# Optimization experiments

Hardware: AMD Instinct MI355X
Metric: run time of the kernel (lower is better)

Reference implementation:

```python
import jax, jax.numpy as jnp
import numpy as np

IN_CH, OUT_CH, K, STRIDE, PAD = 256, 256, 3, 1, 1

# Straight-through-estimator sign (torch Binarize: sign fwd, identity bwd)
@jax.custom_vjp
def ste_sign(x):
    return jnp.sign(x)

def _ste_fwd(x):
    return jnp.sign(x), None

def _ste_bwd(_, g):
    return (g,)

ste_sign.defvjp(_ste_fwd, _ste_bwd)


def setup_inputs() -> dict:
    key = jax.random.key(0)
    ks = jax.random.split(key, 4)
    x = jax.random.normal(ks[0], (32, IN_CH, 56, 56), jnp.float32)
    shift1 = jnp.zeros((1, IN_CH, 1, 1), jnp.float32)
    shift2 = jnp.zeros((1, IN_CH, 1, 1), jnp.float32)
    fan_in = IN_CH * K * K
    weight = jax.random.normal(ks[1], (OUT_CH, IN_CH, K, K), jnp.float32) / np.sqrt(fan_in)
    bias = jax.random.normal(ks[2], (OUT_CH,), jnp.float32) * 0.01
    w1 = jax.random.uniform(ks[3], (1,), jnp.float32) * 0.001  # channel_w scalar
    return {"x": x, "shift1": shift1, "shift2": shift2,
            "weight": weight, "bias": bias, "w1": w1}


def _binarize_conv2d(x, weight, bias):
    # BinarizeConv2d: binarize input (in_ch != 3) and weight via sign, fp conv, add bias
    xb = ste_sign(x)
    wb = ste_sign(weight)
    out = jax.lax.conv_general_dilated(
        xb, wb,
        window_strides=(STRIDE, STRIDE),
        padding=[(PAD, PAD), (PAD, PAD)],
        dimension_numbers=("NCHW", "OIHW", "NCHW"))
    return out + bias[None, :, None, None]


def reference(x, shift1, shift2, weight, bias, w1):
    out1 = _binarize_conv2d(x + shift1, weight, bias)
    out2 = _binarize_conv2d(x + shift2, weight, bias)
    return out1 + w1 * out2
```

## Files before the change

### kernel.cpp

```cpp
#include <hip/hip_runtime.h>
#include <stdint.h>

typedef __attribute__((ext_vector_type(4))) int   i32x4v;
typedef __attribute__((ext_vector_type(16))) int  i32x16v;
typedef __attribute__((ext_vector_type(4))) float f32x4;

#define PIX 3136
#define WW 56
#define SPL 53824
#define SLAB 215296
#define ABUF 16384
#define EPQ (32*69*4)
#define LDSB 65536

#define XBP_BYTES ((size_t)32*4*215296)
#define OFF_XBP2  (XBP_BYTES)
#define OFF_WBT   (2*XBP_BYTES)
#define WBT_BYTES ((size_t)9*16*256*16)
#define OFF_FLAG  (OFF_WBT + WBT_BYTES)
#define WS_NEED   (OFF_FLAG + 64)

__global__ __launch_bounds__(256) void k_prep(
    const float* __restrict__ s1, const float* __restrict__ s2,
    const float* __restrict__ w, char* __restrict__ ws,
    char* __restrict__ wbTt, int* __restrict__ flag) {
    int b = blockIdx.x;
    int t = threadIdx.x;
    if (b == 0) {
        __shared__ int bad;
        if (t == 0) bad = 0;
        __syncthreads();
        if (s1[t] != s2[t]) atomicAdd(&bad, 1);
        __syncthreads();
        if (t == 0) *flag = (bad == 0) ? 1 : 0;
        return;
    }
    if (b <= 256) {
        char* base = ws + (size_t)(b - 1) * SLAB;
        int4 z = {0, 0, 0, 0};
#pragma unroll
        for (int i = 0; i < 4; ++i) {
            int u = t + i * 256;
            if (u >= 912) break;
            int s = u / 228, v = u - s * 228;
            int off;
            if (v < 58)       off = v;
            else if (v < 116) off = 3306 + (v - 58);
            else { int r = v - 116; off = ((r >> 1) + 1) * 58 + (r & 1) * 57; }
            *(int4*)(base + s * SPL + off * 16) = z;
        }
        return;
    }
    int idx = (b - 257) * 256 + t;
    int kk = idx >> 16;
    int sub = (idx >> 12) & 15;
    int oc = (idx >> 4) & 255;
    int lo = idx & 15;
    float v = w[(oc * 256 + sub * 16 + lo) * 9 + kk];
    wbTt[idx] = (v > 0.f) ? (char)1 : ((v < 0.f) ? (char)-1 : (char)0);
}

__global__ __launch_bounds__(256) void k_repack_x(
    const float* __restrict__ x, const float* __restrict__ sh1,
    const float* __restrict__ sh2, char* __restrict__ xbp1,
    char* __restrict__ xbp2, const int* __restrict__ flag) {
    __shared__ float lds[64 * 68];
    bool eq = (*flag != 0);
    int t = threadIdx.x;
    int b = blockIdx.x;
    int n = b / 49;
    int p0 = (b % 49) * 64;

    int pixw = t >> 2;
    int sub  = t & 3;
    int pw = p0 + pixw;
    int yw = pw / WW, xw = pw % WW;

    int cl = t >> 4;
    int p4 = (t & 15) * 4;

    for (int cc = 0; cc < 256; cc += 64) {
        __syncthreads();
#pragma unroll
        for (int i = 0; i < 4; ++i) {
            float4 v = *(const float4*)(x + (size_t)(n * 256 + cc + cl + i * 16) * PIX + p0 + p4);
            *(float4*)(&lds[(cl + i * 16) * 68 + p4]) = v;
        }
        __syncthreads();
        size_t obase = (size_t)(n * 4 + (cc >> 6)) * SLAB + (size_t)sub * SPL
                     + ((size_t)(yw + 1) * 58 + (xw + 1)) * 16;
        union { char c[16]; int4 v; } u1, u2;
#pragma unroll
        for (int k = 0; k < 16; ++k) {
            int c = sub * 16 + k;
            float v = lds[c * 68 + pixw];
            float a1 = v + sh1[cc + c];
            float a2 = v + sh2[cc + c];
            u1.c[k] = (a1 > 0.f) ? (char)1 : ((a1 < 0.f) ? (char)-1 : (char)0);
            u2.c[k] = (a2 > 0.f) ? (char)1 : ((a2 < 0.f) ? (char)-1 : (char)0);
        }
        *(int4*)(xbp1 + obase) = u1.v;
        if (!eq) *(int4*)(xbp2 + obase) = u2.v;
    }
}

template <int MODE>
__global__ __launch_bounds__(256, 2) void k_bgemm(
    const char* __restrict__ xsrc, const char* __restrict__ wbTt,
    const float* __restrict__ bias, const float* __restrict__ w1,
    const int* __restrict__ flag, float* __restrict__ out) {
    bool eq = (*flag != 0);
    if (MODE == 0 ? !eq : eq) return;

    __shared__ char lds[LDSB];

    int t = threadIdx.x;
    int l = t & 63, wid = t >> 6;
    int r32 = l & 31, half = l >> 5;

    int logical = (blockIdx.x & 7) * 196 + (blockIdx.x >> 3);
    int n = logical / 49, tp = logical % 49;
    int p0 = tp * 64;
    int y0 = p0 / WW;
    int ocw = wid * 64;

    int wpm[2];
#pragma unroll
    for (int mi = 0; mi < 2; ++mi) {
        int g = p0 + mi * 32 + r32;
        int yg = g / WW, xg = g - yg * WW;
        wpm[mi] = (yg + 1 - y0) * 58 + xg + 1;
    }

    auto stageB = [&](int par, int t2) {
        const int cc2 = t2 / 9, kk2 = t2 % 9;
        const char* src = wbTt + kk2 * 65536 + cc2 * 16384 + wid * 4096 + l * 16;
        char* dst = lds + 32768 + par * 16384 + wid * 4096;
#pragma unroll
        for (int j = 0; j < 4; ++j)
            __builtin_amdgcn_global_load_lds(
                (const __attribute__((address_space(1))) void*)(src + j * 1024),
                (__attribute__((address_space(3))) void*)(dst + j * 1024), 16, 0, 0);
    };
    auto stageA = [&](int par, int cc2) {
        const char* src = xsrc + (size_t)(n * 4 + cc2) * SLAB + (size_t)wid * SPL
                        + y0 * 928 + l * 16;
        char* dst = lds + par * ABUF + wid * 4096;
#pragma unroll
        for (int j = 0; j < 4; ++j)
            __builtin_amdgcn_global_load_lds(
                (const __attribute__((address_space(1))) void*)(src + j * 1024),
                (__attribute__((address_space(3))) void*)(dst + j * 1024), 16, 0, 0);
    };

    i32x16v acc[2][2];
#pragma unroll
    for (int mi = 0; mi < 2; ++mi)
#pragma unroll
        for (int nj = 0; nj < 2; ++nj)
#pragma unroll
            for (int i = 0; i < 16; ++i) acc[mi][nj][i] = 0;

    stageA(0, 0);
    stageB(0, 0);
    __syncthreads();

#pragma unroll
    for (int tix = 0; tix < 36; ++tix) {
        const int cc = tix / 9, kk = tix % 9;
        if (tix < 35) stageB((tix + 1) & 1, tix + 1);
        if (kk == 4 && cc < 3) stageA((cc + 1) & 1, cc + 1);
        const int ts = (kk / 3 - 1) * 58 + (kk % 3) - 1;
        const char* Ab = lds + (cc & 1) * ABUF;
        const char* Bb = lds + 32768 + (tix & 1) * 16384;
#pragma unroll
        for (int kq = 0; kq < 2; ++kq) {
            const int ci = kq * 2 + half;
            i32x4v af0 = *(const i32x4v*)(Ab + ci * 4096 + (wpm[0] + ts) * 16);
            i32x4v af1 = *(const i32x4v*)(Ab + ci * 4096 + (wpm[1] + ts) * 16);
            i32x4v bf0 = *(const i32x4v*)(Bb + ci * 4096 + (ocw + r32) * 16);
            i32x4v bf1 = *(const i32x4v*)(Bb + ci * 4096 + (ocw + 32 + r32) * 16);
            acc[0][0] = __builtin_amdgcn_mfma_i32_32x32x32_i8(af0, bf0, acc[0][0], 0, 0, 0);
            acc[0][1] = __builtin_amdgcn_mfma_i32_32x32x32_i8(af0, bf1, acc[0][1], 0, 0, 0);
            acc[1][0] = __builtin_amdgcn_mfma_i32_32x32x32_i8(af1, bf0, acc[1][0], 0, 0, 0);
            acc[1][1] = __builtin_amdgcn_mfma_i32_32x32x32_i8(af1, bf1, acc[1][1], 0, 0, 0);
        }
        __syncthreads();
    }

    float w1v = w1[0];
    float se = 1.f + w1v;
    float* sb = (float*)(lds + wid * EPQ);
    size_t outb = (size_t)n * 256 * PIX + p0;

#pragma unroll
    for (int nj = 0; nj < 2; ++nj) {
        float bv = bias[ocw + nj * 32 + r32];
#pragma unroll
        for (int mi = 0; mi < 2; ++mi)
#pragma unroll
            for (int q = 0; q < 4; ++q) {
                f32x4 v;
#pragma unroll
                for (int j = 0; j < 4; ++j) {
                    float a = (float)(acc[mi][nj][q * 4 + j]);
                    if (MODE == 0)      v[j] = (a + bv) * se;
                    else if (MODE == 1) v[j] = a + se * bv;
                    else                v[j] = w1v * a;
                }
                *(f32x4*)(sb + r32 * 69 + mi * 32 + q * 8 + half * 4) = v;
            }
        asm volatile("s_waitcnt lgkmcnt(0)" ::: "memory");
#pragma unroll
        for (int p = 0; p < 8; ++p) {
            int row = p * 4 + (l >> 4);
            int px4 = (l & 15) * 4;
            f32x4 v = *(const f32x4*)(sb + row * 69 + px4);
            float* op = out + outb + (size_t)(ocw + nj * 32 + row) * PIX + px4;
            if (MODE == 2) {
                f32x4 o = *(const f32x4*)op;
                v[0] += o[0]; v[1] += o[1]; v[2] += o[2]; v[3] += o[3];
            }
            __builtin_nontemporal_store(v, (f32x4*)op);
        }
        if (nj == 0) asm volatile("s_waitcnt lgkmcnt(0)" ::: "memory");
    }
}

extern "C" void kernel_launch(void* const* d_in, const int* in_sizes, int n_in,
                              void* d_out, int out_size, void* d_ws, size_t ws_size,
                              hipStream_t stream) {
    const float* x    = (const float*)d_in[0];
    const float* sh1  = (const float*)d_in[1];
    const float* sh2  = (const float*)d_in[2];
    const float* wgt  = (const float*)d_in[3];
    const float* bias = (const float*)d_in[4];
    const float* w1   = (const float*)d_in[5];
    float* out = (float*)d_out;
    char* ws = (char*)d_ws;
    if (ws_size < WS_NEED) return;

    char* xbp1 = ws;
    char* xbp2 = ws + OFF_XBP2;
    char* wbTt = ws + OFF_WBT;
    int* flag  = (int*)(ws + OFF_FLAG);

    k_prep<<<2561, 256, 0, stream>>>(sh1, sh2, wgt, ws, wbTt, flag);
    k_repack_x<<<32 * 49, 256, 0, stream>>>(x, sh1, sh2, xbp1, xbp2, flag);
    k_bgemm<0><<<1568, 256, 0, stream>>>(xbp1, wbTt, bias, w1, flag, out);
    k_bgemm<1><<<1568, 256, 0, stream>>>(xbp1, wbTt, bias, w1, flag, out);
    k_bgemm<2><<<1568, 256, 0, stream>>>(xbp2, wbTt, bias, w1, flag, out);
}
```

Before: 116.6 us.

## Retile binary conv GEMM to 128px x 128oc blocks with single A buffer

Changes the block tile from 64 pixels x 256 output channels to 128 pixels x 128 channels, with 4 waves arranged 2x2, and uses 1600 blocks with clamped tails. The A (input) slab is now single-buffered and reloaded between channel chunks behind an extra barrier. B staging is halved, so LDS per block falls to about 37KB, which lets launch bounds target 3 blocks per CU. The aim is higher occupancy and better reuse balance, at the cost of exposed A-load latency at each chunk boundary and some wasted work on the padded last pixel tile.

Result: faster. 105.5 us (-9.6%).

```diff
diff --git a/kernel.cpp b/kernel.cpp
--- a/kernel.cpp
+++ b/kernel.cpp
@@ -9,9 +9,10 @@
 #define WW 56
 #define SPL 53824
 #define SLAB 215296
-#define ABUF 16384
+#define APL 5184
+#define ABASE 16384
 #define EPQ (32*69*4)
-#define LDSB 65536
+#define LDSB 37120
 
 #define XBP_BYTES ((size_t)32*4*215296)
 #define OFF_XBP2  (XBP_BYTES)
@@ -105,7 +106,7 @@
 }
 
 template <int MODE>
-__global__ __launch_bounds__(256, 2) void k_bgemm(
+__global__ __launch_bounds__(256, 3) void k_bgemm(
     const char* __restrict__ xsrc, const char* __restrict__ wbTt,
     const float* __restrict__ bias, const float* __restrict__ w1,
     const int* __restrict__ flag, float* __restrict__ out) {
@@ -116,38 +117,46 @@
 
     int t = threadIdx.x;
     int l = t & 63, wid = t >> 6;
+    int wr = wid >> 1, wc = wid & 1;
     int r32 = l & 31, half = l >> 5;
 
-    int logical = (blockIdx.x & 7) * 196 + (blockIdx.x >> 3);
-    int n = logical / 49, tp = logical % 49;
-    int p0 = tp * 64;
+    int logical = (blockIdx.x & 7) * 200 + (blockIdx.x >> 3);
+    int ntile = logical & 1;
+    int m = logical >> 1;
+    int n = m / 25, tp = m % 25;
+    int p0 = tp * 128;
     int y0 = p0 / WW;
-    int ocw = wid * 64;
+    int y0c = (y0 < 53) ? y0 : 53;
+    int ocb = ntile * 128 + wc * 64;
+    int pxb = p0 + wr * 64;
+    bool pvalid = pxb < PIX;
 
     int wpm[2];
 #pragma unroll
     for (int mi = 0; mi < 2; ++mi) {
-        int g = p0 + mi * 32 + r32;
+        int g = pxb + mi * 32 + r32;
+        if (g > 3135) g = 3135;
         int yg = g / WW, xg = g - yg * WW;
-        wpm[mi] = (yg + 1 - y0) * 58 + xg + 1;
+        wpm[mi] = (yg + 1 - y0c) * 58 + xg + 1;
     }
 
     auto stageB = [&](int par, int t2) {
         const int cc2 = t2 / 9, kk2 = t2 % 9;
-        const char* src = wbTt + kk2 * 65536 + cc2 * 16384 + wid * 4096 + l * 16;
-        char* dst = lds + 32768 + par * 16384 + wid * 4096;
-#pragma unroll
-        for (int j = 0; j < 4; ++j)
+        const char* src = wbTt
+            + ((size_t)((kk2 * 16 + cc2 * 4 + wid) * 256 + ntile * 128)) * 16 + l * 16;
+        char* dst = lds + par * 8192 + wid * 2048;
+#pragma unroll
+        for (int j = 0; j < 2; ++j)
             __builtin_amdgcn_global_load_lds(
                 (const __attribute__((address_space(1))) void*)(src + j * 1024),
                 (__attribute__((address_space(3))) void*)(dst + j * 1024), 16, 0, 0);
     };
-    auto stageA = [&](int par, int cc2) {
+    auto stageA = [&](int cc2) {
         const char* src = xsrc + (size_t)(n * 4 + cc2) * SLAB + (size_t)wid * SPL
-                        + y0 * 928 + l * 16;
-        char* dst = lds + par * ABUF + wid * 4096;
-#pragma unroll
-        for (int j = 0; j < 4; ++j)
+                        + y0c * 928 + l * 16;
+        char* dst = lds + ABASE + wid * APL;
+#pragma unroll
+        for (int j = 0; j < 5; ++j)
             __builtin_amdgcn_global_load_lds(
                 (const __attribute__((address_space(1))) void*)(src + j * 1024),
                 (__attribute__((address_space(3))) void*)(dst + j * 1024), 16, 0, 0);
@@ -161,41 +170,47 @@
 #pragma unroll
             for (int i = 0; i < 16; ++i) acc[mi][nj][i] = 0;
 
-    stageA(0, 0);
+    stageA(0);
     stageB(0, 0);
     __syncthreads();
 
 #pragma unroll
-    for (int tix = 0; tix < 36; ++tix) {
-        const int cc = tix / 9, kk = tix % 9;
-        if (tix < 35) stageB((tix + 1) & 1, tix + 1);
-        if (kk == 4 && cc < 3) stageA((cc + 1) & 1, cc + 1);
-        const int ts = (kk / 3 - 1) * 58 + (kk % 3) - 1;
-        const char* Ab = lds + (cc & 1) * ABUF;
-        const char* Bb = lds + 32768 + (tix & 1) * 16384;
-#pragma unroll
-        for (int kq = 0; kq < 2; ++kq) {
-            const int ci = kq * 2 + half;
-            i32x4v af0 = *(const i32x4v*)(Ab + ci * 4096 + (wpm[0] + ts) * 16);
-            i32x4v af1 = *(const i32x4v*)(Ab + ci * 4096 + (wpm[1] + ts) * 16);
-            i32x4v bf0 = *(const i32x4v*)(Bb + ci * 4096 + (ocw + r32) * 16);
-            i32x4v bf1 = *(const i32x4v*)(Bb + ci * 4096 + (ocw + 32 + r32) * 16);
-            acc[0][0] = __builtin_amdgcn_mfma_i32_32x32x32_i8(af0, bf0, acc[0][0], 0, 0, 0);
-            acc[0][1] = __builtin_amdgcn_mfma_i32_32x32x32_i8(af0, bf1, acc[0][1], 0, 0, 0);
-            acc[1][0] = __builtin_amdgcn_mfma_i32_32x32x32_i8(af1, bf0, acc[1][0], 0, 0, 0);
-            acc[1][1] = __builtin_amdgcn_mfma_i32_32x32x32_i8(af1, bf1, acc[1][1], 0, 0, 0);
-        }
-        __syncthreads();
+    for (int cc = 0; cc < 4; ++cc) {
+#pragma unroll
+        for (int kk = 0; kk < 9; ++kk) {
+            const int tix = cc * 9 + kk;
+            if (tix < 35) stageB((tix + 1) & 1, tix + 1);
+            const int ts = (kk / 3 - 1) * 58 + (kk % 3) - 1;
+            const char* Ab = lds + ABASE;
+            const char* Bb = lds + (tix & 1) * 8192;
+#pragma unroll
+            for (int kq = 0; kq < 2; ++kq) {
+                const int ci = kq * 2 + half;
+                i32x4v af0 = *(const i32x4v*)(Ab + ci * APL + (wpm[0] + ts) * 16);
+                i32x4v af1 = *(const i32x4v*)(Ab + ci * APL + (wpm[1] + ts) * 16);
+                i32x4v bf0 = *(const i32x4v*)(Bb + ci * 2048 + (wc * 64 + r32) * 16);
+                i32x4v bf1 = *(const i32x4v*)(Bb + ci * 2048 + (wc * 64 + 32 + r32) * 16);
+                acc[0][0] = __builtin_amdgcn_mfma_i32_32x32x32_i8(af0, bf0, acc[0][0], 0, 0, 0);
+                acc[0][1] = __builtin_amdgcn_mfma_i32_32x32x32_i8(af0, bf1, acc[0][1], 0, 0, 0);
+                acc[1][0] = __builtin_amdgcn_mfma_i32_32x32x32_i8(af1, bf0, acc[1][0], 0, 0, 0);
+                acc[1][1] = __builtin_amdgcn_mfma_i32_32x32x32_i8(af1, bf1, acc[1][1], 0, 0, 0);
+            }
+            __syncthreads();
+        }
+        if (cc < 3) {
+            stageA(cc + 1);
+            __syncthreads();
+        }
     }
 
     float w1v = w1[0];
     float se = 1.f + w1v;
     float* sb = (float*)(lds + wid * EPQ);
-    size_t outb = (size_t)n * 256 * PIX + p0;
+    size_t outb = (size_t)n * 256 * PIX + pxb;
 
 #pragma unroll
     for (int nj = 0; nj < 2; ++nj) {
-        float bv = bias[ocw + nj * 32 + r32];
+        float bv = bias[ocb + nj * 32 + r32];
 #pragma unroll
         for (int mi = 0; mi < 2; ++mi)
 #pragma unroll
@@ -211,17 +226,19 @@
                 *(f32x4*)(sb + r32 * 69 + mi * 32 + q * 8 + half * 4) = v;
             }
         asm volatile("s_waitcnt lgkmcnt(0)" ::: "memory");
-#pragma unroll
-        for (int p = 0; p < 8; ++p) {
-            int row = p * 4 + (l >> 4);
-            int px4 = (l & 15) * 4;
-            f32x4 v = *(const f32x4*)(sb + row * 69 + px4);
-            float* op = out + outb + (size_t)(ocw + nj * 32 + row) * PIX + px4;
-            if (MODE == 2) {
-                f32x4 o = *(const f32x4*)op;
-                v[0] += o[0]; v[1] += o[1]; v[2] += o[2]; v[3] += o[3];
+        if (pvalid) {
+#pragma unroll
+            for (int p = 0; p < 8; ++p) {
+                int row = p * 4 + (l >> 4);
+                int px4 = (l & 15) * 4;
+                f32x4 v = *(const f32x4*)(sb + row * 69 + px4);
+                float* op = out + outb + (size_t)(ocb + nj * 32 + row) * PIX + px4;
+                if (MODE == 2) {
+                    f32x4 o = *(const f32x4*)op;
+                    v[0] += o[0]; v[1] += o[1]; v[2] += o[2]; v[3] += o[3];
+                }
+                __builtin_nontemporal_store(v, (f32x4*)op);
             }
-            __builtin_nontemporal_store(v, (f32x4*)op);
         }
         if (nj == 0) asm volatile("s_waitcnt lgkmcnt(0)" ::: "memory");
     }
@@ -247,7 +264,7 @@
 
     k_prep<<<2561, 256, 0, stream>>>(sh1, sh2, wgt, ws, wbTt, flag);
     k_repack_x<<<32 * 49, 256, 0, stream>>>(x, sh1, sh2, xbp1, xbp2, flag);
-    k_bgemm<0><<<1568, 256, 0, stream>>>(xbp1, wbTt, bias, w1, flag, out);
-    k_bgemm<1><<<1568, 256, 0, stream>>>(xbp1, wbTt, bias, w1, flag, out);
-    k_bgemm<2><<<1568, 256, 0, stream>>>(xbp2, wbTt, bias, w1, flag, out);
-}
+    k_bgemm<0><<<1600, 256, 0, stream>>>(xbp1, wbTt, bias, w1, flag, out);
+    k_bgemm<1><<<1600, 256, 0, stream>>>(xbp1, wbTt, bias, w1, flag, out);
+    k_bgemm<2><<<1600, 256, 0, stream>>>(xbp2, wbTt, bias, w1, flag, out);
+}
```
